# Kernel tuning notes

Hardware: AMD Instinct MI355X
Metric: run time of the kernel (lower is better)

## Reference

```python
import jax, jax.numpy as jnp
import numpy as np

N = 2048
H_DIM = 64
N_HEADS = 4
N_HIDDEN = H_DIM // N_HEADS  # is_concat=True
L = 16  # max_labels_dim
SLOPE = 0.2


def leaky(x, slope=SLOPE):
    return jnp.where(x >= 0, x, slope * x)


def setup_inputs() -> dict:
    key = jax.random.key(0)
    k1, k2, k3, k4 = jax.random.split(key, 4)
    x = jax.random.normal(k1, (N, H_DIM), dtype=jnp.float32)
    # labels in [0, L]; value == L means unlabeled -> all-zero one-hot row
    lab = jax.random.randint(k2, (N,), 0, L + 1)
    ohm_labels = jnp.where((lab < L)[:, None],
                           jax.nn.one_hot(jnp.minimum(lab, L - 1), L, dtype=jnp.float32),
                           0.0)
    in_features = H_DIM + L
    W_l = jax.random.normal(k3, (H_DIM, in_features), dtype=jnp.float32) / np.sqrt(in_features)
    W_attn = jax.random.normal(k4, (N_HIDDEN,), dtype=jnp.float32) / np.sqrt(N_HIDDEN)
    return {"x": x, "ohm_labels": ohm_labels, "W_l": W_l, "W_attn": W_attn, "sparsity": 0}


def reference(x, ohm_labels, W_l, W_attn, sparsity):
    n_nodes = x.shape[0]
    # fill unlabeled rows with uniform 1/L
    unlabeled = ohm_labels.sum(axis=1) == 0  # (N,)
    ohm = jnp.where(unlabeled[:, None], 1.0 / L, ohm_labels)
    pin = jnp.concatenate([x, ohm], axis=1)  # (N, h_dim + L)

    # shared-weight projection: g_l == g_r == g
    g = (pin @ W_l.T).reshape(n_nodes, N_HEADS, N_HIDDEN)  # (N, H, F)
    # g_sum[i, j] = g_l[j] + g_r[i]  (repeat / repeat_interleave semantics)
    g_sum = g[None, :, :, :] + g[:, None, :, :]            # (N, N, H, F)
    e = jnp.einsum('ijhf,f->ijh', leaky(g_sum), W_attn)    # (N, N, H)
    a = jax.nn.softmax(e, axis=1)                          # softmax over j
    # dropout in eval mode: identity
    attn_res = jnp.einsum('ijh,jhf->ihf', a, g)            # (N, H, F)
    out = attn_res.reshape(n_nodes, N_HEADS * N_HIDDEN)    # is_concat
    h = leaky(out)                                         # processor activation

    # centroids per label from ohm (post-fill) as in get_centroids
    cluster_agg = ohm.T @ h                                # (L, D)
    cnt = ohm.sum(axis=0)                                  # (L,)
    missing = cnt == 0
    centroids = jnp.where(missing[:, None], 0.0,
                          cluster_agg / jnp.where(missing, 1.0, cnt)[:, None])
    # cdist p=2
    diff = h[:, None, :] - centroids[None, :, :]           # (N, L, D)
    scores = -jnp.sqrt(jnp.sum(diff * diff, axis=-1))      # (N, L)
    return scores, h, missing
```

## Files before the change

kernel.cpp:

```cpp
#include <hip/hip_runtime.h>
#include <hip/hip_bf16.h>
#include <math.h>

#define C1F  0.577078016f
#define C2F  0.865617024f

#define WS_CNT 0
#define WS_AGG 128
#define WS_G   8320
#define WS_DCL (8320 + 524288)

typedef float __attribute__((ext_vector_type(4))) f32x4;

__device__ __forceinline__ float dpp_sum(float x) {
    float y;
    y = __int_as_float(__builtin_amdgcn_update_dpp(0, __float_as_int(x), 0x111, 0xf, 0xf, true)); x += y;
    y = __int_as_float(__builtin_amdgcn_update_dpp(0, __float_as_int(x), 0x112, 0xf, 0xf, true)); x += y;
    y = __int_as_float(__builtin_amdgcn_update_dpp(0, __float_as_int(x), 0x114, 0xf, 0xf, true)); x += y;
    y = __int_as_float(__builtin_amdgcn_update_dpp(0, __float_as_int(x), 0x118, 0xf, 0xf, true)); x += y;
    y = __int_as_float(__builtin_amdgcn_update_dpp(0, __float_as_int(x), 0x142, 0xa, 0xf, true)); x += y;
    y = __int_as_float(__builtin_amdgcn_update_dpp(0, __float_as_int(x), 0x143, 0xc, 0xf, true)); x += y;
    return x;
}

__global__ __launch_bounds__(256) void k_proj(
    const float* __restrict__ x, const float* __restrict__ ohm,
    const float* __restrict__ Wl, const float* __restrict__ Wattn,
    unsigned char* __restrict__ ws)
{
    float* g   = (float*)(ws + WS_G);
    float* dcl = (float*)(ws + WS_DCL);
    unsigned long long* cnt = (unsigned long long*)(ws + WS_CNT);

    int t = threadIdx.x;
    int r = blockIdx.x * 4 + (t >> 6);
    int o = t & 63;

    f32x4 oh[4]; float rs = 0.f;
    const f32x4* ohp = (const f32x4*)&ohm[r*16];
    #pragma unroll
    for (int q = 0; q < 4; ++q) { oh[q] = ohp[q]; rs += oh[q][0]+oh[q][1]+oh[q][2]+oh[q][3]; }
    if (rs == 0.f) {
        f32x4 c = {0.0625f, 0.0625f, 0.0625f, 0.0625f};
        #pragma unroll
        for (int q = 0; q < 4; ++q) oh[q] = c;
    }

    float acc = 0.f;
    const f32x4* xp = (const f32x4*)&x[r*64];
    const f32x4* wp = (const f32x4*)&Wl[o*80];
    #pragma unroll
    for (int q = 0; q < 16; ++q) {
        f32x4 a = xp[q], b = wp[q];
        acc = fmaf(a[0],b[0],acc); acc = fmaf(a[1],b[1],acc);
        acc = fmaf(a[2],b[2],acc); acc = fmaf(a[3],b[3],acc);
    }
    #pragma unroll
    for (int q = 0; q < 4; ++q) {
        f32x4 b = wp[16+q];
        acc = fmaf(oh[q][0],b[0],acc); acc = fmaf(oh[q][1],b[1],acc);
        acc = fmaf(oh[q][2],b[2],acc); acc = fmaf(oh[q][3],b[3],acc);
    }
    g[r*64 + o] = acc;

    float dot = Wattn[o & 15] * acc;
    #pragma unroll
    for (int m2 = 1; m2 < 16; m2 <<= 1) dot += __shfl_xor(dot, m2);
    if ((o & 15) == 0) dcl[r*4 + (o >> 4)] = C2F * dot;

    if (t < 16) {
        float c = 0.f;
        for (int rr = 0; rr < 4; ++rr) {
            int r2 = blockIdx.x*4 + rr; float s = 0.f;
            #pragma unroll
            for (int k = 0; k < 16; ++k) s += ohm[r2*16+k];
            c += (s == 0.f) ? 0.0625f : ohm[r2*16+t];
        }
        atomicAdd(&cnt[t], (unsigned long long)__float2ll_rn(c * 1048576.0f));
    }
}

__global__ __launch_bounds__(512, 4) void k_attn(
    const float* __restrict__ ohm, const float* __restrict__ Wattn,
    unsigned char* __restrict__ ws, float* __restrict__ hout)
{
    float* g   = (float*)(ws + WS_G);
    float* dcl = (float*)(ws + WS_DCL);
    unsigned long long* agg = (unsigned long long*)(ws + WS_AGG);

    __shared__ float gl[2][128*68];
    __shared__ float shh[256];
    __shared__ float ohmf[64];

    int t = threadIdx.x, bid = blockIdx.x;
    int wid = t >> 6, l = t & 63;
    int ipair = wid >> 2, h = wid & 3;
    int iA = bid*4 + ipair*2, iB = iA + 1;

    const f32x4* gsrc = (const f32x4*)(g) + t*4;
    float* wd0 = &gl[0][(t >> 2)*68 + (t & 3)*16];
    float* wd1 = &gl[1][(t >> 2)*68 + (t & 3)*16];

    float wv[16], gA[16], gB[16];
    #pragma unroll
    for (int f = 0; f < 16; ++f)
        wv[f] = __uint_as_float(__builtin_amdgcn_readfirstlane(__float_as_uint(Wattn[f])));
    #pragma unroll
    for (int f = 0; f < 16; ++f) {
        gA[f] = g[iA*64 + h*16 + f];
        gB[f] = g[iB*64 + h*16 + f];
    }
    float accA[16], accB[16];
    #pragma unroll
    for (int f = 0; f < 16; ++f) { accA[f] = 0.f; accB[f] = 0.f; }
    float lA = 0.f, lB = 0.f;

    const float* dp = dcl + (l*4 + h);

    f32x4 s0a = gsrc[0], s0b = gsrc[1], s0c = gsrc[2], s0d = gsrc[3];
    f32x4 s1a = gsrc[2048+0], s1b = gsrc[2048+1], s1c = gsrc[2048+2], s1d = gsrc[2048+3];
    float djc0 = dp[0],   djc1 = dp[256];
    float djn0 = dp[512], djn1 = dp[768];
    *(f32x4*)(wd0+0) = s0a; *(f32x4*)(wd0+4)  = s0b;
    *(f32x4*)(wd0+8) = s0c; *(f32x4*)(wd0+12) = s0d;
    f32x4 sta = s1a, stb = s1b, stc = s1c, std_ = s1d;
    asm volatile("s_waitcnt lgkmcnt(0)\n\ts_barrier" ::: "memory");

    #pragma unroll
    for (int tile = 0; tile < 16; ++tile) {
        if (tile < 15) {
            float* wd = (tile & 1) ? wd0 : wd1;
            *(f32x4*)(wd+0) = sta;  *(f32x4*)(wd+4)  = stb;
            *(f32x4*)(wd+8) = stc;  *(f32x4*)(wd+12) = std_;
        }
        float djn2_0 = 0.f, djn2_1 = 0.f;
        if (tile < 14) {
            const f32x4* src2 = gsrc + (tile+2)*2048;
            sta = src2[0]; stb = src2[1]; stc = src2[2]; std_ = src2[3];
            djn2_0 = dp[(tile+2)*512]; djn2_1 = dp[(tile+2)*512 + 256];
        }

        const float* bp = (tile & 1) ? &gl[1][0] : &gl[0][0];
        #pragma unroll
        for (int kk = 0; kk < 2; ++kk) {
            float djk = kk ? djc1 : djc0;
            const float* gj = bp + (kk*64 + l)*68 + h*16;
            f32x4 q0 = *(const f32x4*)(gj);
            f32x4 q1 = *(const f32x4*)(gj+4);
            f32x4 q2 = *(const f32x4*)(gj+8);
            f32x4 q3 = *(const f32x4*)(gj+12);
            float gv[16] = { q0[0],q0[1],q0[2],q0[3], q1[0],q1[1],q1[2],q1[3],
                             q2[0],q2[1],q2[2],q2[3], q3[0],q3[1],q3[2],q3[3] };
            float sA0=0.f, sA1=0.f, sB0=0.f, sB1=0.f;
            #pragma unroll
            for (int f = 0; f < 16; f += 2) {
                float ta0 = gA[f]   + gv[f];
                float ta1 = gA[f+1] + gv[f+1];
                float tb0 = gB[f]   + gv[f];
                float tb1 = gB[f+1] + gv[f+1];
                sA0 = fmaf(wv[f],   fabsf(ta0), sA0);
                sA1 = fmaf(wv[f+1], fabsf(ta1), sA1);
                sB0 = fmaf(wv[f],   fabsf(tb0), sB0);
                sB1 = fmaf(wv[f+1], fabsf(tb1), sB1);
            }
            float pA = __builtin_amdgcn_exp2f(fmaf(C1F, sA0 + sA1, djk));
            float pB = __builtin_amdgcn_exp2f(fmaf(C1F, sB0 + sB1, djk));
            lA += pA; lB += pB;
            #pragma unroll
            for (int f = 0; f < 16; ++f) {
                accA[f] = fmaf(pA, gv[f], accA[f]);
                accB[f] = fmaf(pB, gv[f], accB[f]);
            }
        }
        asm volatile("s_waitcnt lgkmcnt(0)\n\ts_barrier" ::: "memory");
        djc0 = djn0; djc1 = djn1;
        djn0 = djn2_0; djn1 = djn2_1;
    }

    float lAs = dpp_sum(lA), lBs = dpp_sum(lB);
    float hA[16], hB[16];
    #pragma unroll
    for (int f = 0; f < 16; ++f) { hA[f] = dpp_sum(accA[f]); hB[f] = dpp_sum(accB[f]); }

    if (l == 63) {
        float rA = 1.0f / lAs, rB = 1.0f / lBs;
        #pragma unroll
        for (int f = 0; f < 16; ++f) {
            float a = hA[f]*rA; a = fmaxf(a, 0.2f*a);
            float b = hB[f]*rB; b = fmaxf(b, 0.2f*b);
            hout[iA*64 + h*16 + f] = a;
            hout[iB*64 + h*16 + f] = b;
            shh[(ipair*2    )*64 + h*16 + f] = a;
            shh[(ipair*2 + 1)*64 + h*16 + f] = b;
        }
    }
    if (t < 64) {
        int rr = t >> 4, ll = t & 15;
        float v = ohm[(bid*4 + rr)*16 + ll];
        float s = v;
        #pragma unroll
        for (int m2 = 1; m2 < 16; m2 <<= 1) s += __shfl_xor(s, m2);
        ohmf[rr*16 + ll] = (s == 0.f) ? 0.0625f : v;
    }
    __syncthreads();

    for (int v = t; v < 1024; v += 512) {
        int ll = v >> 6, d = v & 63;
        float s = 0.f;
        #pragma unroll
        for (int rr = 0; rr < 4; ++rr) s = fmaf(ohmf[rr*16 + ll], shh[rr*64 + d], s);
        atomicAdd(&agg[v], (unsigned long long)__float2ll_rn(s * 67108864.0f));
    }
}

__global__ __launch_bounds__(256) void k_scores(
    unsigned char* __restrict__ ws, const float* __restrict__ hout,
    float* __restrict__ scores, float* __restrict__ missing)
{
    __shared__ float cl[16*68];
    unsigned long long* cnt = (unsigned long long*)(ws + WS_CNT);
    unsigned long long* agg = (unsigned long long*)(ws + WS_AGG);
    int t = threadIdx.x;

    for (int v = t; v < 1024; v += 256) {
        int ll = v >> 6, d = v & 63;
        long long a = (long long)agg[v];
        long long c = (long long)cnt[ll];
        cl[ll*68 + d] = (c == 0) ? 0.f : ((float)a / (float)c) * 0.015625f;
    }
    if (blockIdx.x == 0 && t < 16) missing[t] = (cnt[t] == 0) ? 1.0f : 0.0f;
    __syncthreads();

    int i = blockIdx.x*16 + (t >> 4), ll = t & 15;
    float s = 0.f;
    #pragma unroll 16
    for (int d = 0; d < 64; ++d) {
        float diff = hout[i*64 + d] - cl[ll*68 + d];
        s = fmaf(diff, diff, s);
    }
    scores[i*16 + ll] = -sqrtf(s);
}

extern "C" void kernel_launch(void* const* d_in, const int* in_sizes, int n_in,
                              void* d_out, int out_size, void* d_ws, size_t ws_size,
                              hipStream_t stream)
{
    const float* x     = (const float*)d_in[0];
    const float* ohm   = (const float*)d_in[1];
    const float* Wl    = (const float*)d_in[2];
    const float* Wattn = (const float*)d_in[3];
    unsigned char* ws  = (unsigned char*)d_ws;

    float* out     = (float*)d_out;
    float* scores  = out;
    float* hout    = out + 2048*16;
    float* missing = out + 2048*16 + 2048*64;

    hipMemsetAsync(d_ws, 0, 8320, stream);
    k_proj  <<<512, 256, 0, stream>>>(x, ohm, Wl, Wattn, ws);
    k_attn  <<<512, 512, 0, stream>>>(ohm, Wattn, ws, hout);
    k_scores<<<128, 256, 0, stream>>>(ws, hout, scores, missing);
}
```

Before: 61.05 us.

## Remap attention work to 32-lane groups per row-head with transposed dcl layout

Each 32-lane half-wave now handles one output row and head, iterating four j-columns per tile, instead of each wave handling two rows with one column per lane. The dcl array is stored transposed (head-major) so the per-j loads are contiguous, and the final reduction drops one DPP step to sum over 32 lanes. This changes register pressure and work per thread, aiming for better balance and lower accumulator cost. In exchange, loaded g values are reused across one row instead of two, so LDS read traffic per FLOP doubles.

```diff
diff --git a/kernel.cpp b/kernel.cpp
--- a/kernel.cpp
+++ b/kernel.cpp
@@ -12,14 +12,13 @@
 
 typedef float __attribute__((ext_vector_type(4))) f32x4;
 
-__device__ __forceinline__ float dpp_sum(float x) {
+__device__ __forceinline__ float dpp_sum32(float x) {
     float y;
     y = __int_as_float(__builtin_amdgcn_update_dpp(0, __float_as_int(x), 0x111, 0xf, 0xf, true)); x += y;
     y = __int_as_float(__builtin_amdgcn_update_dpp(0, __float_as_int(x), 0x112, 0xf, 0xf, true)); x += y;
     y = __int_as_float(__builtin_amdgcn_update_dpp(0, __float_as_int(x), 0x114, 0xf, 0xf, true)); x += y;
     y = __int_as_float(__builtin_amdgcn_update_dpp(0, __float_as_int(x), 0x118, 0xf, 0xf, true)); x += y;
     y = __int_as_float(__builtin_amdgcn_update_dpp(0, __float_as_int(x), 0x142, 0xa, 0xf, true)); x += y;
-    y = __int_as_float(__builtin_amdgcn_update_dpp(0, __float_as_int(x), 0x143, 0xc, 0xf, true)); x += y;
     return x;
 }
 
@@ -28,8 +27,8 @@
     const float* __restrict__ Wl, const float* __restrict__ Wattn,
     unsigned char* __restrict__ ws)
 {
-    float* g   = (float*)(ws + WS_G);
-    float* dcl = (float*)(ws + WS_DCL);
+    float* g    = (float*)(ws + WS_G);
+    float* dclT = (float*)(ws + WS_DCL);
     unsigned long long* cnt = (unsigned long long*)(ws + WS_CNT);
 
     int t = threadIdx.x;
@@ -66,7 +65,7 @@
     float dot = Wattn[o & 15] * acc;
     #pragma unroll
     for (int m2 = 1; m2 < 16; m2 <<= 1) dot += __shfl_xor(dot, m2);
-    if ((o & 15) == 0) dcl[r*4 + (o >> 4)] = C2F * dot;
+    if ((o & 15) == 0) dclT[(o >> 4)*2048 + r] = C2F * dot;
 
     if (t < 16) {
         float c = 0.f;
@@ -84,8 +83,8 @@
     const float* __restrict__ ohm, const float* __restrict__ Wattn,
     unsigned char* __restrict__ ws, float* __restrict__ hout)
 {
-    float* g   = (float*)(ws + WS_G);
-    float* dcl = (float*)(ws + WS_DCL);
+    float* g    = (float*)(ws + WS_G);
+    float* dclT = (float*)(ws + WS_DCL);
     unsigned long long* agg = (unsigned long long*)(ws + WS_AGG);
 
     __shared__ float gl[2][128*68];
@@ -93,105 +92,92 @@
     __shared__ float ohmf[64];
 
     int t = threadIdx.x, bid = blockIdx.x;
-    int wid = t >> 6, l = t & 63;
-    int ipair = wid >> 2, h = wid & 3;
-    int iA = bid*4 + ipair*2, iB = iA + 1;
-
-    const f32x4* gsrc = (const f32x4*)(g) + t*4;
-    float* wd0 = &gl[0][(t >> 2)*68 + (t & 3)*16];
-    float* wd1 = &gl[1][(t >> 2)*68 + (t & 3)*16];
-
-    float wv[16], gA[16], gB[16];
+    int p = t >> 5, sub = t & 31;
+    int r = p >> 2, h = p & 3;
+    int irow = bid*4 + r;
+
+    const f32x4* gv4 = (const f32x4*)g;
+    float* w0 = &gl[0][(t >> 4)*68 + (t & 15)*4];
+    float* w1 = &gl[1][(t >> 4)*68 + (t & 15)*4];
+
+    float wv[16], gA[16];
     #pragma unroll
     for (int f = 0; f < 16; ++f)
         wv[f] = __uint_as_float(__builtin_amdgcn_readfirstlane(__float_as_uint(Wattn[f])));
     #pragma unroll
-    for (int f = 0; f < 16; ++f) {
-        gA[f] = g[iA*64 + h*16 + f];
-        gB[f] = g[iB*64 + h*16 + f];
-    }
-    float accA[16], accB[16];
-    #pragma unroll
-    for (int f = 0; f < 16; ++f) { accA[f] = 0.f; accB[f] = 0.f; }
-    float lA = 0.f, lB = 0.f;
-
-    const float* dp = dcl + (l*4 + h);
-
-    f32x4 s0a = gsrc[0], s0b = gsrc[1], s0c = gsrc[2], s0d = gsrc[3];
-    f32x4 s1a = gsrc[2048+0], s1b = gsrc[2048+1], s1c = gsrc[2048+2], s1d = gsrc[2048+3];
-    float djc0 = dp[0],   djc1 = dp[256];
-    float djn0 = dp[512], djn1 = dp[768];
-    *(f32x4*)(wd0+0) = s0a; *(f32x4*)(wd0+4)  = s0b;
-    *(f32x4*)(wd0+8) = s0c; *(f32x4*)(wd0+12) = s0d;
-    f32x4 sta = s1a, stb = s1b, stc = s1c, std_ = s1d;
+    for (int f = 0; f < 16; ++f) gA[f] = g[irow*64 + h*16 + f];
+
+    float acc[16];
+    #pragma unroll
+    for (int f = 0; f < 16; ++f) acc[f] = 0.f;
+    float lsum = 0.f;
+
+    const float* dpt = dclT + h*2048 + sub;
+
+    f32x4 s0[4], st[4];
+    float djc[4], djn[4], djn2[4] = {0.f,0.f,0.f,0.f};
+    #pragma unroll
+    for (int q = 0; q < 4; ++q) { s0[q] = gv4[t + q*512]; st[q] = gv4[2048 + t + q*512]; }
+    #pragma unroll
+    for (int k = 0; k < 4; ++k) { djc[k] = dpt[k*32]; djn[k] = dpt[128 + k*32]; }
+    #pragma unroll
+    for (int q = 0; q < 4; ++q) *(f32x4*)(w0 + q*2176) = s0[q];
     asm volatile("s_waitcnt lgkmcnt(0)\n\ts_barrier" ::: "memory");
 
     #pragma unroll
     for (int tile = 0; tile < 16; ++tile) {
         if (tile < 15) {
-            float* wd = (tile & 1) ? wd0 : wd1;
-            *(f32x4*)(wd+0) = sta;  *(f32x4*)(wd+4)  = stb;
-            *(f32x4*)(wd+8) = stc;  *(f32x4*)(wd+12) = std_;
-        }
-        float djn2_0 = 0.f, djn2_1 = 0.f;
+            float* wd = (tile & 1) ? w0 : w1;
+            #pragma unroll
+            for (int q = 0; q < 4; ++q) *(f32x4*)(wd + q*2176) = st[q];
+        }
         if (tile < 14) {
-            const f32x4* src2 = gsrc + (tile+2)*2048;
-            sta = src2[0]; stb = src2[1]; stc = src2[2]; std_ = src2[3];
-            djn2_0 = dp[(tile+2)*512]; djn2_1 = dp[(tile+2)*512 + 256];
+            #pragma unroll
+            for (int q = 0; q < 4; ++q) st[q] = gv4[(tile+2)*2048 + t + q*512];
+            #pragma unroll
+            for (int k = 0; k < 4; ++k) djn2[k] = dpt[(tile+2)*128 + k*32];
         }
 
         const float* bp = (tile & 1) ? &gl[1][0] : &gl[0][0];
         #pragma unroll
-        for (int kk = 0; kk < 2; ++kk) {
-            float djk = kk ? djc1 : djc0;
-            const float* gj = bp + (kk*64 + l)*68 + h*16;
+        for (int k = 0; k < 4; ++k) {
+            const float* gj = bp + (k*32 + sub)*68 + h*16;
             f32x4 q0 = *(const f32x4*)(gj);
             f32x4 q1 = *(const f32x4*)(gj+4);
             f32x4 q2 = *(const f32x4*)(gj+8);
             f32x4 q3 = *(const f32x4*)(gj+12);
-            float gv[16] = { q0[0],q0[1],q0[2],q0[3], q1[0],q1[1],q1[2],q1[3],
-                             q2[0],q2[1],q2[2],q2[3], q3[0],q3[1],q3[2],q3[3] };
-            float sA0=0.f, sA1=0.f, sB0=0.f, sB1=0.f;
+            float gvv[16] = { q0[0],q0[1],q0[2],q0[3], q1[0],q1[1],q1[2],q1[3],
+                              q2[0],q2[1],q2[2],q2[3], q3[0],q3[1],q3[2],q3[3] };
+            float s0a = 0.f, s1a = 0.f;
             #pragma unroll
             for (int f = 0; f < 16; f += 2) {
-                float ta0 = gA[f]   + gv[f];
-                float ta1 = gA[f+1] + gv[f+1];
-                float tb0 = gB[f]   + gv[f];
-                float tb1 = gB[f+1] + gv[f+1];
-                sA0 = fmaf(wv[f],   fabsf(ta0), sA0);
-                sA1 = fmaf(wv[f+1], fabsf(ta1), sA1);
-                sB0 = fmaf(wv[f],   fabsf(tb0), sB0);
-                sB1 = fmaf(wv[f+1], fabsf(tb1), sB1);
+                float t0 = gA[f]   + gvv[f];
+                float t1 = gA[f+1] + gvv[f+1];
+                s0a = fmaf(wv[f],   fabsf(t0), s0a);
+                s1a = fmaf(wv[f+1], fabsf(t1), s1a);
             }
-            float pA = __builtin_amdgcn_exp2f(fmaf(C1F, sA0 + sA1, djk));
-            float pB = __builtin_amdgcn_exp2f(fmaf(C1F, sB0 + sB1, djk));
-            lA += pA; lB += pB;
-            #pragma unroll
-            for (int f = 0; f < 16; ++f) {
-                accA[f] = fmaf(pA, gv[f], accA[f]);
-                accB[f] = fmaf(pB, gv[f], accB[f]);
-            }
+            float pj = __builtin_amdgcn_exp2f(fmaf(C1F, s0a + s1a, djc[k]));
+            lsum += pj;
+            #pragma unroll
+            for (int f = 0; f < 16; ++f) acc[f] = fmaf(pj, gvv[f], acc[f]);
         }
         asm volatile("s_waitcnt lgkmcnt(0)\n\ts_barrier" ::: "memory");
-        djc0 = djn0; djc1 = djn1;
-        djn0 = djn2_0; djn1 = djn2_1;
-    }
-
-    float lAs = dpp_sum(lA), lBs = dpp_sum(lB);
-    float hA[16], hB[16];
-    #pragma unroll
-    for (int f = 0; f < 16; ++f) { hA[f] = dpp_sum(accA[f]); hB[f] = dpp_sum(accB[f]); }
-
-    if (l == 63) {
-        float rA = 1.0f / lAs, rB = 1.0f / lBs;
+        #pragma unroll
+        for (int k = 0; k < 4; ++k) { djc[k] = djn[k]; djn[k] = djn2[k]; }
+    }
+
+    float ls = dpp_sum32(lsum);
+    float hv[16];
+    #pragma unroll
+    for (int f = 0; f < 16; ++f) hv[f] = dpp_sum32(acc[f]);
+
+    if ((t & 31) == 31) {
+        float rl = 1.0f / ls;
         #pragma unroll
         for (int f = 0; f < 16; ++f) {
-            float a = hA[f]*rA; a = fmaxf(a, 0.2f*a);
-            float b = hB[f]*rB; b = fmaxf(b, 0.2f*b);
-            hout[iA*64 + h*16 + f] = a;
-            hout[iB*64 + h*16 + f] = b;
-            shh[(ipair*2    )*64 + h*16 + f] = a;
-            shh[(ipair*2 + 1)*64 + h*16 + f] = b;
+            float a = hv[f]*rl; a = fmaxf(a, 0.2f*a);
+            hout[irow*64 + h*16 + f] = a;
+            shh[r*64 + h*16 + f] = a;
         }
     }
     if (t < 64) {
```

Result: faster. 57.74 us (-5.4%).
